# Optimization experiments

Hardware: AMD Instinct MI355X
Metric: run time of the kernel (lower is better)

The kernel has to match this reference:

```python
import jax, jax.numpy as jnp
from jax import lax
import numpy as np

B, L, V, E, D, T = 512, 200, 50000, 256, 256, 6
H = D // 2          # per-direction LSTM hidden
SLOPE = 0.01        # LeakyReLU negative slope
START, STOP = 4, 5  # tag_map['START'], tag_map['STOP']


def setup_inputs():
    key = jax.random.key(0)
    ks = jax.random.split(key, 18)
    w = lambda k, shape, scale=0.05: jax.random.normal(k, shape, jnp.float32) * scale
    trans = jax.random.normal(ks[17], (T, T), jnp.float32)
    trans = trans.at[:, START].set(-1000.0)
    trans = trans.at[STOP, :].set(-1000.0)
    return {
        "sentences": jax.random.randint(ks[0], (B, L), 0, V),
        "real_length": jnp.full((B,), L, dtype=jnp.int32),
        "emb": jax.random.normal(ks[1], (V, E), jnp.float32),
        "Wih_f": w(ks[2], (4 * H, E)), "Whh_f": w(ks[3], (4 * H, H)),
        "bih_f": w(ks[4], (4 * H,)),   "bhh_f": w(ks[5], (4 * H,)),
        "Wih_b": w(ks[6], (4 * H, E)), "Whh_b": w(ks[7], (4 * H, H)),
        "bih_b": w(ks[8], (4 * H,)),   "bhh_b": w(ks[9], (4 * H,)),
        "W1": w(ks[10], (D, D)), "b1": w(ks[11], (D,)),
        "W2": w(ks[12], (D, D)), "b2": w(ks[13], (D,)),
        "Wt": w(ks[14], (T, D)), "bt": w(ks[15], (T,)),
        "transitions": trans,
    }


def _leaky(x):
    return jnp.where(x >= 0, x, SLOPE * x)


def _lstm_dir(x, Wih, Whh, bih, bhh):
    # x: [B, L, E] -> hidden states [B, L, H]; PyTorch gate order i,f,g,o
    Bn = x.shape[0]
    Hn = Whh.shape[1]
    xg = jnp.einsum('ble,ge->blg', x, Wih) + bih + bhh  # [B, L, 4H]
    def step(carry, xt):
        h, c = carry
        g = xt + h @ Whh.T
        i, f, gg, o = jnp.split(g, 4, axis=-1)
        c = jax.nn.sigmoid(f) * c + jax.nn.sigmoid(i) * jnp.tanh(gg)
        h = jax.nn.sigmoid(o) * jnp.tanh(c)
        return (h, c), h
    init = (jnp.zeros((Bn, Hn), x.dtype), jnp.zeros((Bn, Hn), x.dtype))
    _, hs = lax.scan(step, init, jnp.swapaxes(xg, 0, 1))  # [L, B, H]
    return jnp.swapaxes(hs, 0, 1)


def _emissions(sentences, emb, Wih_f, Whh_f, bih_f, bhh_f, Wih_b, Whh_b, bih_b, bhh_b,
               W1, b1, W2, b2, Wt, bt):
    x = emb[sentences]                                   # [B, L, E]
    hf = _lstm_dir(x, Wih_f, Whh_f, bih_f, bhh_f)
    hb = _lstm_dir(x[:, ::-1], Wih_b, Whh_b, bih_b, bhh_b)[:, ::-1]
    h = jnp.concatenate([hf, hb], axis=-1)               # [B, L, D]
    h = _leaky(h @ W1.T + b1)
    h = _leaky(h @ W2.T + b2)
    return _leaky(h @ Wt.T + bt)                         # [B, L, T]


def _viterbi(logits, transitions):
    # logits: [L, T]; trellis recursion then backtrace
    def step(prev, obs):
        v = prev[:, None] + transitions                  # [T, T]
        tr = obs + jnp.max(v, axis=0)
        return tr, jnp.argmax(v, axis=0)
    last, bps = lax.scan(step, logits[0], logits[1:])    # bps: [L-1, T]
    score = jnp.max(last)
    last_tag = jnp.argmax(last)
    def back(tag, bp):
        new = bp[tag]
        return new, new
    _, prevs = lax.scan(back, last_tag, bps[::-1])
    path = jnp.concatenate([prevs[::-1], last_tag[None]])  # [L]
    return score, path


def reference(sentences, real_length, emb, Wih_f, Whh_f, bih_f, bhh_f,
              Wih_b, Whh_b, bih_b, bhh_b, W1, b1, W2, b2, Wt, bt, transitions):
    # real_length is full (=L) for every sample, so pack/pad is the identity,
    # matching the original forward's lengths=[i.size(-1)] behavior.
    logits = _emissions(sentences, emb, Wih_f, Whh_f, bih_f, bhh_f,
                        Wih_b, Whh_b, bih_b, bhh_b, W1, b1, W2, b2, Wt, bt)
    scores, paths = jax.vmap(_viterbi, in_axes=(0, None))(logits, transitions)
    return scores, paths
```

## Files before the change

### kernel.cpp

```cpp
#include <hip/hip_runtime.h>
#include <cmath>

#define B_   512
#define L_   200
#define V_   50000
#define E_   256
#define H_   128
#define G4H_ 512
#define D_   256
#define T_   6

__device__ __forceinline__ float sigmoidf_(float x) { return 1.0f / (1.0f + __expf(-x)); }
__device__ __forceinline__ float leakyf_(float x)   { return x >= 0.0f ? x : 0.01f * x; }

template<int CTRL>
__device__ __forceinline__ float dpp_add_(float x) {
    const int m = __builtin_amdgcn_mov_dpp(__float_as_int(x), CTRL, 0xF, 0xF, true);
    return x + __int_as_float(m);
}

#define XBM 128
#define XBN 128
#define XBK 8
#define XSTR 132

__global__ __launch_bounds__(256) void gemm_xg_chunk(
    const int* __restrict__ sent, const float* __restrict__ emb,
    const float* __restrict__ Wf, const float* __restrict__ Wb,
    const float* __restrict__ bihf, const float* __restrict__ bhhf,
    const float* __restrict__ bihb, const float* __restrict__ bhhb,
    float* __restrict__ xgc, int c0, int tc)
{
    __shared__ float As[2][XBK][XSTR];
    __shared__ float Bs[2][XBK][XSTR];
    __shared__ int   tok[XBM];

    const int bm  = blockIdx.x;
    const int bn  = blockIdx.y;
    const int tid = threadIdx.x;
    const int half = B_ * tc;
    const int dir  = (bm * XBM) >= half;

    if (tid < XBM) {
        const int vm  = bm * XBM + tid;
        const int rem = vm - dir * half;
        const int b   = rem / tc;
        const int ti  = rem - b * tc;
        const int s   = c0 + ti;
        const int t   = dir ? (L_ - 1 - s) : s;
        tok[tid] = sent[b * L_ + t];
    }
    __syncthreads();

    const int tx = tid & 15;
    const int ty = tid >> 4;
    const int n0 = bn * XBN;

    const float* W   = dir ? Wb   : Wf;
    const float* bih = dir ? bihb : bihf;
    const float* bhh = dir ? bhhb : bhhf;

    const int am = tid >> 1;
    const int ak = (tid & 1) * 4;

    const float* arow = emb + (size_t)tok[am] * E_ + ak;
    const float* brow = W + (size_t)(n0 + am) * E_ + ak;

    float acc[8][8];
#pragma unroll
    for (int i = 0; i < 8; ++i)
#pragma unroll
        for (int j = 0; j < 8; ++j) acc[i][j] = 0.0f;

    {
        const float4 a = *(const float4*)(arow);
        const float4 b = *(const float4*)(brow);
        As[0][ak + 0][am] = a.x; As[0][ak + 1][am] = a.y;
        As[0][ak + 2][am] = a.z; As[0][ak + 3][am] = a.w;
        Bs[0][ak + 0][am] = b.x; Bs[0][ak + 1][am] = b.y;
        Bs[0][ak + 2][am] = b.z; Bs[0][ak + 3][am] = b.w;
    }
    __syncthreads();

    const int NIT = E_ / XBK;
    for (int it = 0; it < NIT; ++it) {
        const int cur = it & 1;
        const int kn  = (it + 1) * XBK;
        float4 na, nb;
        if (kn < E_) {
            na = *(const float4*)(arow + kn);
            nb = *(const float4*)(brow + kn);
        }
#pragma unroll
        for (int k = 0; k < XBK; ++k) {
            float a[8], bb[8];
            *(float4*)a        = *(const float4*)&As[cur][k][ty * 4];
            *(float4*)(a + 4)  = *(const float4*)&As[cur][k][64 + ty * 4];
            *(float4*)(bb)     = *(const float4*)&Bs[cur][k][tx * 4];
            *(float4*)(bb + 4) = *(const float4*)&Bs[cur][k][64 + tx * 4];
#pragma unroll
            for (int i = 0; i < 8; ++i)
#pragma unroll
                for (int j = 0; j < 8; ++j) acc[i][j] += a[i] * bb[j];
        }
        if (kn < E_) {
            const int nxt = cur ^ 1;
            As[nxt][ak + 0][am] = na.x; As[nxt][ak + 1][am] = na.y;
            As[nxt][ak + 2][am] = na.z; As[nxt][ak + 3][am] = na.w;
            Bs[nxt][ak + 0][am] = nb.x; Bs[nxt][ak + 1][am] = nb.y;
            Bs[nxt][ak + 2][am] = nb.z; Bs[nxt][ak + 3][am] = nb.w;
        }
        __syncthreads();
    }

    const int nb0i = n0 + tx * 4;
    const int nb1i = n0 + 64 + tx * 4;
    float bias[8];
#pragma unroll
    for (int j = 0; j < 4; ++j) {
        bias[j]     = bih[nb0i + j] + bhh[nb0i + j];
        bias[4 + j] = bih[nb1i + j] + bhh[nb1i + j];
    }
#pragma unroll
    for (int i = 0; i < 8; ++i) {
        const int row = bm * XBM + ((i < 4) ? (ty * 4 + i) : (64 + ty * 4 + i - 4));
        float* dst = xgc + (size_t)row * G4H_;
        float4 v0, v1;
        v0.x = acc[i][0] + bias[0]; v0.y = acc[i][1] + bias[1];
        v0.z = acc[i][2] + bias[2]; v0.w = acc[i][3] + bias[3];
        v1.x = acc[i][4] + bias[4]; v1.y = acc[i][5] + bias[5];
        v1.z = acc[i][6] + bias[6]; v1.w = acc[i][7] + bias[7];
        *(float4*)(dst + nb0i) = v0;
        *(float4*)(dst + nb1i) = v1;
    }
}

__global__ __launch_bounds__(512, 2) void lstm_scan_chunk(
    const float* __restrict__ xgc,
    const float* __restrict__ Whh_f, const float* __restrict__ Whh_b,
    float* __restrict__ state, float* __restrict__ hcat, int c0, int tc)
{
    const int wg  = blockIdx.x;
    const int dir = wg >> 7;
    const int b0  = (wg & 127) * 4;
    const int tid = threadIdx.x;

    const int q  = tid & 3;
    const int g2 = tid >> 2;

    const float* Whh = dir ? Whh_b : Whh_f;

    float w[4][32];
#pragma unroll
    for (int p = 0; p < 4; ++p) {
        const float* wr = Whh + (size_t)(g2 + 128 * p) * H_ + q * 32;
#pragma unroll
        for (int kk = 0; kk < 32; kk += 4) {
            const float4 v = *(const float4*)(wr + kk);
            w[p][kk] = v.x; w[p][kk + 1] = v.y; w[p][kk + 2] = v.z; w[p][kk + 3] = v.w;
        }
    }

    __shared__ float hbuf[2][4 * 132];

    float c, hval;
    if (c0 == 0) {
        hval = 0.0f;
        c    = 0.0f;
    } else {
        hval = state[((size_t)(dir * B_ + b0 + q) * 2 + 0) * H_ + g2];
        c    = state[((size_t)(dir * B_ + b0 + q) * 2 + 1) * H_ + g2];
    }
    hbuf[0][(g2 >> 5) * 132 + (g2 & 31) * 4 + q] = hval;

    const int t0    = dir ? (L_ - 1 - c0) : c0;
    const int hstep = dir ? -D_ : D_;

    const float* xq = xgc + ((size_t)(dir * B_ + b0 + q) * tc) * G4H_ + g2;
    float* hp = hcat + ((size_t)(b0 + q) * L_ + t0) * D_ + dir * H_ + g2;

    __syncthreads();

    for (int t = 0; t < tc; ++t) {
        const int par = t & 1;
        const float* hq = &hbuf[par][q * 132];

        float xg[4];
#pragma unroll
        for (int p = 0; p < 4; ++p) xg[p] = xq[128 * p];
        xq += G4H_;

        float acc[4][4];
#pragma unroll
        for (int p = 0; p < 4; ++p)
#pragma unroll
            for (int s = 0; s < 4; ++s) acc[p][s] = 0.0f;

#pragma unroll
        for (int kk = 0; kk < 32; ++kk) {
            const float4 hv = *(const float4*)(hq + kk * 4);
#pragma unroll
            for (int p = 0; p < 4; ++p) {
                acc[p][0] += w[p][kk] * hv.x;
                acc[p][1] += w[p][kk] * hv.y;
                acc[p][2] += w[p][kk] * hv.z;
                acc[p][3] += w[p][kk] * hv.w;
            }
        }

#pragma unroll
        for (int p = 0; p < 4; ++p)
#pragma unroll
            for (int s = 0; s < 4; ++s) {
                float v = acc[p][s];
                v = dpp_add_<0xB1>(v);
                v = dpp_add_<0x4E>(v);
                acc[p][s] = v;
            }

        float gi = acc[0][0], gf = acc[1][0], gg = acc[2][0], go = acc[3][0];
        if (q == 1) { gi = acc[0][1]; gf = acc[1][1]; gg = acc[2][1]; go = acc[3][1]; }
        if (q == 2) { gi = acc[0][2]; gf = acc[1][2]; gg = acc[2][2]; go = acc[3][2]; }
        if (q == 3) { gi = acc[0][3]; gf = acc[1][3]; gg = acc[2][3]; go = acc[3][3]; }
        gi += xg[0]; gf += xg[1]; gg += xg[2]; go += xg[3];

        c    = sigmoidf_(gf) * c + sigmoidf_(gi) * tanhf(gg);
        hval = sigmoidf_(go) * tanhf(c);

        hbuf[par ^ 1][(g2 >> 5) * 132 + (g2 & 31) * 4 + q] = hval;
        hp[0] = hval;
        hp += hstep;
        __syncthreads();
    }

    state[((size_t)(dir * B_ + b0 + q) * 2 + 0) * H_ + g2] = hval;
    state[((size_t)(dir * B_ + b0 + q) * 2 + 1) * H_ + g2] = c;
}

#define BM 64
#define BN 128
#define BK 16
#define ASTR 68
#define BSTR 132
#define S1T 68

__global__ __launch_bounds__(256) void fused_mlp(
    const float* __restrict__ hcat,
    const float* __restrict__ W1, const float* __restrict__ b1,
    const float* __restrict__ W2, const float* __restrict__ b2,
    const float* __restrict__ Wt, const float* __restrict__ bt,
    float* __restrict__ logits)
{
    __shared__ float As[BK][ASTR];
    __shared__ float Bs[BK][BSTR];
    __shared__ float h1T[BN][S1T];
    __shared__ float Wt_s[T_][D_ + 2];
    __shared__ float b1_s[D_], b2_s[D_], bt_s[T_];

    const int tid  = threadIdx.x;
    const int row0 = blockIdx.x * BM;

    for (int i = tid; i < T_ * D_; i += 256) Wt_s[i >> 8][i & 255] = Wt[i];
    b1_s[tid] = b1[tid];
    b2_s[tid] = b2[tid];
    if (tid < T_) bt_s[tid] = bt[tid];

    const int tx = tid & 15;
    const int ty = tid >> 4;
    const int lrow = tid >> 2;
    const int lk   = (tid & 3) * 4;

    const float* arow = hcat + (size_t)(row0 + lrow) * D_ + lk;

    float acc2[2][4][8];
#pragma unroll
    for (int q = 0; q < 2; ++q)
#pragma unroll
        for (int i = 0; i < 4; ++i)
#pragma unroll
            for (int j = 0; j < 8; ++j) acc2[q][i][j] = 0.0f;

    for (int n0t = 0; n0t < 2; ++n0t) {
        const int n0 = n0t * BN;

        float acc1[4][8];
#pragma unroll
        for (int i = 0; i < 4; ++i)
#pragma unroll
            for (int j = 0; j < 8; ++j) acc1[i][j] = 0.0f;

        for (int k0 = 0; k0 < D_; k0 += BK) {
            {
                const float4 v = *(const float4*)(arow + k0);
                As[lk + 0][lrow] = v.x; As[lk + 1][lrow] = v.y;
                As[lk + 2][lrow] = v.z; As[lk + 3][lrow] = v.w;
            }
#pragma unroll
            for (int p = 0; p < 2; ++p) {
                const int n = p * 64 + lrow;
                const float4 v = *(const float4*)(W1 + (size_t)(n0 + n) * D_ + k0 + lk);
                Bs[lk + 0][n] = v.x; Bs[lk + 1][n] = v.y;
                Bs[lk + 2][n] = v.z; Bs[lk + 3][n] = v.w;
            }
            __syncthreads();
#pragma unroll
            for (int k = 0; k < BK; ++k) {
                float a[4], bb[8];
                *(float4*)a        = *(const float4*)&As[k][ty * 4];
                *(float4*)(bb)     = *(const float4*)&Bs[k][tx * 4];
                *(float4*)(bb + 4) = *(const float4*)&Bs[k][64 + tx * 4];
#pragma unroll
                for (int i = 0; i < 4; ++i)
#pragma unroll
                    for (int j = 0; j < 8; ++j) acc1[i][j] += a[i] * bb[j];
            }
            __syncthreads();
        }

#pragma unroll
        for (int j = 0; j < 8; ++j) {
            const int nl = (j < 4) ? (tx * 4 + j) : (64 + tx * 4 + j - 4);
            const float bv = b1_s[n0 + nl];
            float4 v;
            v.x = leakyf_(acc1[0][j] + bv);
            v.y = leakyf_(acc1[1][j] + bv);
            v.z = leakyf_(acc1[2][j] + bv);
            v.w = leakyf_(acc1[3][j] + bv);
            *(float4*)&h1T[nl][ty * 4] = v;
        }
        __syncthreads();

#pragma unroll
        for (int n2t = 0; n2t < 2; ++n2t) {
            for (int kc = 0; kc < BN; kc += BK) {
#pragma unroll
                for (int p = 0; p < 2; ++p) {
                    const int n = p * 64 + lrow;
                    const float4 v = *(const float4*)(W2 + (size_t)(n2t * BN + n) * D_ + n0 + kc + lk);
                    Bs[lk + 0][n] = v.x; Bs[lk + 1][n] = v.y;
                    Bs[lk + 2][n] = v.z; Bs[lk + 3][n] = v.w;
                }
                __syncthreads();
#pragma unroll
                for (int k = 0; k < BK; ++k) {
                    float a[4], bb[8];
                    *(float4*)a        = *(const float4*)&h1T[kc + k][ty * 4];
                    *(float4*)(bb)     = *(const float4*)&Bs[k][tx * 4];
                    *(float4*)(bb + 4) = *(const float4*)&Bs[k][64 + tx * 4];
#pragma unroll
                    for (int i = 0; i < 4; ++i)
#pragma unroll
                        for (int j = 0; j < 8; ++j) acc2[n2t][i][j] += a[i] * bb[j];
                }
                __syncthreads();
            }
        }
    }

    float part[4][T_];
#pragma unroll
    for (int i = 0; i < 4; ++i)
#pragma unroll
        for (int jt = 0; jt < T_; ++jt) part[i][jt] = 0.0f;

#pragma unroll
    for (int q = 0; q < 2; ++q)
#pragma unroll
        for (int j = 0; j < 8; ++j) {
            const int n = q * BN + ((j < 4) ? (tx * 4 + j) : (64 + tx * 4 + j - 4));
            const float bv = b2_s[n];
            float h2v[4];
#pragma unroll
            for (int i = 0; i < 4; ++i) h2v[i] = leakyf_(acc2[q][i][j] + bv);
#pragma unroll
            for (int jt = 0; jt < T_; ++jt) {
                const float wv = Wt_s[jt][n];
#pragma unroll
                for (int i = 0; i < 4; ++i) part[i][jt] += h2v[i] * wv;
            }
        }

#pragma unroll
    for (int m = 1; m <= 8; m <<= 1)
#pragma unroll
        for (int i = 0; i < 4; ++i)
#pragma unroll
            for (int jt = 0; jt < T_; ++jt)
                part[i][jt] += __shfl_xor(part[i][jt], m, 16);

    if (tx == 0) {
#pragma unroll
        for (int i = 0; i < 4; ++i) {
            const int m = row0 + ty * 4 + i;
#pragma unroll
            for (int jt = 0; jt < T_; ++jt)
                logits[(size_t)m * T_ + jt] = leakyf_(part[i][jt] + bt_s[jt]);
        }
    }
}

__global__ __launch_bounds__(64) void viterbi_kernel(
    const float* __restrict__ logits, const float* __restrict__ trans,
    float* __restrict__ out)
{
    const int b = blockIdx.x;
    const int lane = threadIdx.x;

    __shared__ unsigned char bp[L_][8];
    __shared__ int path_s[L_];

    float tr[T_];
    if (lane < T_) {
#pragma unroll
        for (int i = 0; i < T_; ++i) tr[i] = trans[i * T_ + lane];
    }
    const float* lg = logits + (size_t)b * L_ * T_;
    float prev = (lane < T_) ? lg[lane] : -1e30f;

    for (int t = 1; t < L_; ++t) {
        float m = -1e30f; int arg = 0;
#pragma unroll
        for (int i = 0; i < T_; ++i) {
            const float v = __shfl(prev, i, 64) + tr[i];
            if (v > m) { m = v; arg = i; }
        }
        const float obs = (lane < T_) ? lg[t * T_ + lane] : 0.0f;
        prev = obs + m;
        if (lane < T_) bp[t][lane] = (unsigned char)arg;
    }
    __syncthreads();

    float best = __shfl(prev, 0, 64); int tag = 0;
#pragma unroll
    for (int jj = 1; jj < T_; ++jj) {
        const float v = __shfl(prev, jj, 64);
        if (v > best) { best = v; tag = jj; }
    }
    if (lane == 0) {
        out[b] = best;
        path_s[L_ - 1] = tag;
        for (int t = L_ - 1; t >= 1; --t) {
            tag = bp[t][tag];
            path_s[t - 1] = tag;
        }
    }
    __syncthreads();
    for (int i = lane; i < L_; i += 64)
        out[B_ + (size_t)b * L_ + i] = (float)path_s[i];
}

extern "C" void kernel_launch(void* const* d_in, const int* in_sizes, int n_in,
                              void* d_out, int out_size, void* d_ws, size_t ws_size,
                              hipStream_t stream)
{
    (void)in_sizes; (void)n_in; (void)out_size;

    const int*   sent  = (const int*)  d_in[0];
    const float* emb   = (const float*)d_in[2];
    const float* Wih_f = (const float*)d_in[3];
    const float* Whh_f = (const float*)d_in[4];
    const float* bih_f = (const float*)d_in[5];
    const float* bhh_f = (const float*)d_in[6];
    const float* Wih_b = (const float*)d_in[7];
    const float* Whh_b = (const float*)d_in[8];
    const float* bih_b = (const float*)d_in[9];
    const float* bhh_b = (const float*)d_in[10];
    const float* W1    = (const float*)d_in[11];
    const float* b1    = (const float*)d_in[12];
    const float* W2    = (const float*)d_in[13];
    const float* b2    = (const float*)d_in[14];
    const float* Wt    = (const float*)d_in[15];
    const float* bt    = (const float*)d_in[16];
    const float* trans = (const float*)d_in[17];

    float* ws = (float*)d_ws;
    const size_t HCAT_E = (size_t)B_ * L_ * D_;
    const size_t LG_E   = (size_t)B_ * L_ * T_;
    const size_t ST_E   = (size_t)2 * B_ * 2 * H_;
    float* hcat   = ws;
    float* logits = ws + HCAT_E;
    float* state  = logits + LG_E;
    float* xgc    = state + ST_E;

    const size_t base  = HCAT_E + LG_E + ST_E;
    const size_t per_t = (size_t)2 * B_ * G4H_;
    const size_t ws_f  = ws_size / sizeof(float);
    long long avail = (long long)ws_f - (long long)base;
    int Tc = (avail > 0) ? (int)(avail / (long long)per_t) : 0;
    if (Tc < 1)  Tc = 1;
    if (Tc > L_) Tc = L_;

    float* out = (float*)d_out;

    for (int c0 = 0; c0 < L_; c0 += Tc) {
        const int tc = (L_ - c0 < Tc) ? (L_ - c0) : Tc;
        gemm_xg_chunk<<<dim3(8 * tc, 4), 256, 0, stream>>>(
            sent, emb, Wih_f, Wih_b, bih_f, bhh_f, bih_b, bhh_b, xgc, c0, tc);
        lstm_scan_chunk<<<256, 512, 0, stream>>>(
            xgc, Whh_f, Whh_b, state, hcat, c0, tc);
    }
    fused_mlp<<<(B_ * L_) / BM, 256, 0, stream>>>(
        hcat, W1, b1, W2, b2, Wt, bt, logits);
    viterbi_kernel<<<B_, 64, 0, stream>>>(logits, trans, out);
}
```

Baseline: 1.816 ms.

## Split fused MLP into register-tiled GEMM plus fused second-layer/tag-projection kernel

Replaces the single fused MLP kernel with two kernels when there is enough workspace. The first is a 128x128 double-buffered, 8x8 register-tiled GEMM computing the first layer with bias and LeakyReLU into a scratch buffer that reuses the xg chunk area. The second runs the second layer GEMM and folds in the 6-way tag projection, using shuffle reductions. This trades an extra full-size intermediate write and read for larger, more efficient GEMM tiles. The old fused path is kept as a fallback.

```diff
diff --git a/kernel.cpp b/kernel.cpp
--- a/kernel.cpp
+++ b/kernel.cpp
@@ -235,6 +235,214 @@
 
     state[((size_t)(dir * B_ + b0 + q) * 2 + 0) * H_ + g2] = hval;
     state[((size_t)(dir * B_ + b0 + q) * 2 + 1) * H_ + g2] = c;
+}
+
+__global__ __launch_bounds__(256) void mlp1_gemm(
+    const float* __restrict__ hcat,
+    const float* __restrict__ W1, const float* __restrict__ b1,
+    float* __restrict__ h1)
+{
+    __shared__ float As[2][XBK][XSTR];
+    __shared__ float Bs[2][XBK][XSTR];
+
+    const int bm  = blockIdx.x;
+    const int bn  = blockIdx.y;
+    const int tid = threadIdx.x;
+    const int tx = tid & 15;
+    const int ty = tid >> 4;
+    const int n0 = bn * XBN;
+
+    const int am = tid >> 1;
+    const int ak = (tid & 1) * 4;
+
+    const float* arow = hcat + (size_t)(bm * XBM + am) * D_ + ak;
+    const float* brow = W1 + (size_t)(n0 + am) * D_ + ak;
+
+    float acc[8][8];
+#pragma unroll
+    for (int i = 0; i < 8; ++i)
+#pragma unroll
+        for (int j = 0; j < 8; ++j) acc[i][j] = 0.0f;
+
+    {
+        const float4 a = *(const float4*)(arow);
+        const float4 b = *(const float4*)(brow);
+        As[0][ak + 0][am] = a.x; As[0][ak + 1][am] = a.y;
+        As[0][ak + 2][am] = a.z; As[0][ak + 3][am] = a.w;
+        Bs[0][ak + 0][am] = b.x; Bs[0][ak + 1][am] = b.y;
+        Bs[0][ak + 2][am] = b.z; Bs[0][ak + 3][am] = b.w;
+    }
+    __syncthreads();
+
+    const int NIT = D_ / XBK;
+    for (int it = 0; it < NIT; ++it) {
+        const int cur = it & 1;
+        const int kn  = (it + 1) * XBK;
+        float4 na, nb;
+        if (kn < D_) {
+            na = *(const float4*)(arow + kn);
+            nb = *(const float4*)(brow + kn);
+        }
+#pragma unroll
+        for (int k = 0; k < XBK; ++k) {
+            float a[8], bb[8];
+            *(float4*)a        = *(const float4*)&As[cur][k][ty * 4];
+            *(float4*)(a + 4)  = *(const float4*)&As[cur][k][64 + ty * 4];
+            *(float4*)(bb)     = *(const float4*)&Bs[cur][k][tx * 4];
+            *(float4*)(bb + 4) = *(const float4*)&Bs[cur][k][64 + tx * 4];
+#pragma unroll
+            for (int i = 0; i < 8; ++i)
+#pragma unroll
+                for (int j = 0; j < 8; ++j) acc[i][j] += a[i] * bb[j];
+        }
+        if (kn < D_) {
+            const int nxt = cur ^ 1;
+            As[nxt][ak + 0][am] = na.x; As[nxt][ak + 1][am] = na.y;
+            As[nxt][ak + 2][am] = na.z; As[nxt][ak + 3][am] = na.w;
+            Bs[nxt][ak + 0][am] = nb.x; Bs[nxt][ak + 1][am] = nb.y;
+            Bs[nxt][ak + 2][am] = nb.z; Bs[nxt][ak + 3][am] = nb.w;
+        }
+        __syncthreads();
+    }
+
+    const int nb0i = n0 + tx * 4;
+    const int nb1i = n0 + 64 + tx * 4;
+    float bias[8];
+#pragma unroll
+    for (int j = 0; j < 4; ++j) {
+        bias[j]     = b1[nb0i + j];
+        bias[4 + j] = b1[nb1i + j];
+    }
+#pragma unroll
+    for (int i = 0; i < 8; ++i) {
+        const int row = bm * XBM + ((i < 4) ? (ty * 4 + i) : (64 + ty * 4 + i - 4));
+        float* dst = h1 + (size_t)row * D_;
+        float4 v0, v1;
+        v0.x = leakyf_(acc[i][0] + bias[0]); v0.y = leakyf_(acc[i][1] + bias[1]);
+        v0.z = leakyf_(acc[i][2] + bias[2]); v0.w = leakyf_(acc[i][3] + bias[3]);
+        v1.x = leakyf_(acc[i][4] + bias[4]); v1.y = leakyf_(acc[i][5] + bias[5]);
+        v1.z = leakyf_(acc[i][6] + bias[6]); v1.w = leakyf_(acc[i][7] + bias[7]);
+        *(float4*)(dst + nb0i) = v0;
+        *(float4*)(dst + nb1i) = v1;
+    }
+}
+
+__global__ __launch_bounds__(256) void mlp2tag(
+    const float* __restrict__ h1,
+    const float* __restrict__ W2, const float* __restrict__ b2,
+    const float* __restrict__ Wt, const float* __restrict__ bt,
+    float* __restrict__ logits)
+{
+    __shared__ float As[2][XBK][XSTR];
+    __shared__ float Bs[2][XBK][XSTR];
+    __shared__ float Wt_s[T_][D_ + 2];
+    __shared__ float b2_s[D_];
+    __shared__ float bt_s[T_];
+
+    const int bm  = blockIdx.x;
+    const int tid = threadIdx.x;
+    const int tx = tid & 15;
+    const int ty = tid >> 4;
+
+    for (int i = tid; i < T_ * D_; i += 256) Wt_s[i >> 8][i & 255] = Wt[i];
+    b2_s[tid] = b2[tid];
+    if (tid < T_) bt_s[tid] = bt[tid];
+
+    const int am = tid >> 1;
+    const int ak = (tid & 1) * 4;
+
+    const float* arow = h1 + (size_t)(bm * XBM + am) * D_ + ak;
+
+    float part[8][T_];
+#pragma unroll
+    for (int i = 0; i < 8; ++i)
+#pragma unroll
+        for (int jt = 0; jt < T_; ++jt) part[i][jt] = 0.0f;
+
+    for (int n0t = 0; n0t < 2; ++n0t) {
+        const int n0 = n0t * XBN;
+        const float* brow = W2 + (size_t)(n0 + am) * D_ + ak;
+
+        float acc[8][8];
+#pragma unroll
+        for (int i = 0; i < 8; ++i)
+#pragma unroll
+            for (int j = 0; j < 8; ++j) acc[i][j] = 0.0f;
+
+        {
+            const float4 a = *(const float4*)(arow);
+            const float4 b = *(const float4*)(brow);
+            As[0][ak + 0][am] = a.x; As[0][ak + 1][am] = a.y;
+            As[0][ak + 2][am] = a.z; As[0][ak + 3][am] = a.w;
+            Bs[0][ak + 0][am] = b.x; Bs[0][ak + 1][am] = b.y;
+            Bs[0][ak + 2][am] = b.z; Bs[0][ak + 3][am] = b.w;
+        }
+        __syncthreads();
+
+        const int NIT = D_ / XBK;
+        for (int it = 0; it < NIT; ++it) {
+            const int cur = it & 1;
+            const int kn  = (it + 1) * XBK;
+            float4 na, nb;
+            if (kn < D_) {
+                na = *(const float4*)(arow + kn);
+                nb = *(const float4*)(brow + kn);
+            }
+#pragma unroll
+            for (int k = 0; k < XBK; ++k) {
+                float a[8], bb[8];
+                *(float4*)a        = *(const float4*)&As[cur][k][ty * 4];
+                *(float4*)(a + 4)  = *(const float4*)&As[cur][k][64 + ty * 4];
+                *(float4*)(bb)     = *(const float4*)&Bs[cur][k][tx * 4];
+                *(float4*)(bb + 4) = *(const float4*)&Bs[cur][k][64 + tx * 4];
+#pragma unroll
+                for (int i = 0; i < 8; ++i)
+#pragma unroll
+                    for (int j = 0; j < 8; ++j) acc[i][j] += a[i] * bb[j];
+            }
+            if (kn < D_) {
+                const int nxt = cur ^ 1;
+                As[nxt][ak + 0][am] = na.x; As[nxt][ak + 1][am] = na.y;
+                As[nxt][ak + 2][am] = na.z; As[nxt][ak + 3][am] = na.w;
+                Bs[nxt][ak + 0][am] = nb.x; Bs[nxt][ak + 1][am] = nb.y;
+                Bs[nxt][ak + 2][am] = nb.z; Bs[nxt][ak + 3][am] = nb.w;
+            }
+            __syncthreads();
+        }
+
+#pragma unroll
+        for (int j = 0; j < 8; ++j) {
+            const int col = n0 + ((j < 4) ? (tx * 4 + j) : (64 + tx * 4 + j - 4));
+            const float bv = b2_s[col];
+            float h2v[8];
+#pragma unroll
+            for (int i = 0; i < 8; ++i) h2v[i] = leakyf_(acc[i][j] + bv);
+#pragma unroll
+            for (int jt = 0; jt < T_; ++jt) {
+                const float wv = Wt_s[jt][col];
+#pragma unroll
+                for (int i = 0; i < 8; ++i) part[i][jt] += h2v[i] * wv;
+            }
+        }
+    }
+
+#pragma unroll
+    for (int m = 1; m <= 8; m <<= 1)
+#pragma unroll
+        for (int i = 0; i < 8; ++i)
+#pragma unroll
+            for (int jt = 0; jt < T_; ++jt)
+                part[i][jt] += __shfl_xor(part[i][jt], m, 16);
+
+    if (tx == 0) {
+#pragma unroll
+        for (int i = 0; i < 8; ++i) {
+            const int row = bm * XBM + ((i < 4) ? (ty * 4 + i) : (64 + ty * 4 + i - 4));
+#pragma unroll
+            for (int jt = 0; jt < T_; ++jt)
+                logits[(size_t)row * T_ + jt] = leakyf_(part[i][jt] + bt_s[jt]);
+        }
+    }
 }
 
 #define BM 64
@@ -477,6 +685,7 @@
     const size_t HCAT_E = (size_t)B_ * L_ * D_;
     const size_t LG_E   = (size_t)B_ * L_ * T_;
     const size_t ST_E   = (size_t)2 * B_ * 2 * H_;
+    const size_t H1_E   = HCAT_E;
     float* hcat   = ws;
     float* logits = ws + HCAT_E;
     float* state  = logits + LG_E;
@@ -499,7 +708,14 @@
         lstm_scan_chunk<<<256, 512, 0, stream>>>(
             xgc, Whh_f, Whh_b, state, hcat, c0, tc);
     }
-    fused_mlp<<<(B_ * L_) / BM, 256, 0, stream>>>(
-        hcat, W1, b1, W2, b2, Wt, bt, logits);
+
+    if (avail >= (long long)H1_E) {
+        float* h1 = xgc;
+        mlp1_gemm<<<dim3((B_ * L_) / XBM, 2), 256, 0, stream>>>(hcat, W1, b1, h1);
+        mlp2tag<<<(B_ * L_) / XBM, 256, 0, stream>>>(h1, W2, b2, Wt, bt, logits);
+    } else {
+        fused_mlp<<<(B_ * L_) / BM, 256, 0, stream>>>(
+            hcat, W1, b1, W2, b2, Wt, bt, logits);
+    }
     viterbi_kernel<<<B_, 64, 0, stream>>>(logits, trans, out);
 }
```

After: 1.822 ms. No clear change (+0.3%).

## Split LSTM recurrent dot products across eight lanes using 1024-thread blocks

Applied to the files above, without the earlier changes.

The recurrent scan kernel now splits each gate's 128-element hidden dot product across 8 lanes of 16 elements instead of 4 lanes of 32. Block size doubles to 1024 threads, and an extra DPP half-row mirror step completes the cross-lane reduction. Because the scan is a serial, latency-bound recurrence, halving per-thread FMA work per timestep should shorten each step's critical path. In exchange, the extra reduction step adds cost, half the lanes sit idle during the gate nonlinearities and stores, and the weight register footprint is reshaped.

```diff
diff --git a/kernel.cpp b/kernel.cpp
--- a/kernel.cpp
+++ b/kernel.cpp
@@ -135,7 +135,7 @@
     }
 }
 
-__global__ __launch_bounds__(512, 2) void lstm_scan_chunk(
+__global__ __launch_bounds__(1024) void lstm_scan_chunk(
     const float* __restrict__ xgc,
     const float* __restrict__ Whh_f, const float* __restrict__ Whh_b,
     float* __restrict__ state, float* __restrict__ hcat, int c0, int tc)
@@ -145,49 +145,50 @@
     const int b0  = (wg & 127) * 4;
     const int tid = threadIdx.x;
 
-    const int q  = tid & 3;
-    const int g2 = tid >> 2;
+    const int e   = tid & 7;
+    const int g2  = tid >> 3;
+    const int sx  = e & 3;
 
     const float* Whh = dir ? Whh_b : Whh_f;
 
-    float w[4][32];
+    float w[4][16];
 #pragma unroll
     for (int p = 0; p < 4; ++p) {
-        const float* wr = Whh + (size_t)(g2 + 128 * p) * H_ + q * 32;
-#pragma unroll
-        for (int kk = 0; kk < 32; kk += 4) {
+        const float* wr = Whh + (size_t)(g2 + 128 * p) * H_ + e * 16;
+#pragma unroll
+        for (int kk = 0; kk < 16; kk += 4) {
             const float4 v = *(const float4*)(wr + kk);
             w[p][kk] = v.x; w[p][kk + 1] = v.y; w[p][kk + 2] = v.z; w[p][kk + 3] = v.w;
         }
     }
 
-    __shared__ float hbuf[2][4 * 132];
-
-    float c, hval;
-    if (c0 == 0) {
-        hval = 0.0f;
-        c    = 0.0f;
-    } else {
-        hval = state[((size_t)(dir * B_ + b0 + q) * 2 + 0) * H_ + g2];
-        c    = state[((size_t)(dir * B_ + b0 + q) * 2 + 1) * H_ + g2];
-    }
-    hbuf[0][(g2 >> 5) * 132 + (g2 & 31) * 4 + q] = hval;
+    __shared__ float hbuf[2][8 * 68];
+
+    float c = 0.0f, hval = 0.0f;
+    if (e < 4) {
+        if (c0 != 0) {
+            hval = state[((size_t)(dir * B_ + b0 + e) * 2 + 0) * H_ + g2];
+            c    = state[((size_t)(dir * B_ + b0 + e) * 2 + 1) * H_ + g2];
+        }
+        hbuf[0][(g2 >> 4) * 68 + (g2 & 15) * 4 + e] = hval;
+    }
 
     const int t0    = dir ? (L_ - 1 - c0) : c0;
     const int hstep = dir ? -D_ : D_;
 
-    const float* xq = xgc + ((size_t)(dir * B_ + b0 + q) * tc) * G4H_ + g2;
-    float* hp = hcat + ((size_t)(b0 + q) * L_ + t0) * D_ + dir * H_ + g2;
+    const float* xq = xgc + ((size_t)(dir * B_ + b0 + sx) * tc) * G4H_ + g2;
+    float* hp = hcat + ((size_t)(b0 + sx) * L_ + t0) * D_ + dir * H_ + g2;
 
     __syncthreads();
 
     for (int t = 0; t < tc; ++t) {
         const int par = t & 1;
-        const float* hq = &hbuf[par][q * 132];
-
-        float xg[4];
-#pragma unroll
-        for (int p = 0; p < 4; ++p) xg[p] = xq[128 * p];
+        const float* hq = &hbuf[par][e * 68];
+
+        float xg0 = 0.f, xg1 = 0.f, xg2v = 0.f, xg3 = 0.f;
+        if (e < 4) {
+            xg0 = xq[0]; xg1 = xq[128]; xg2v = xq[256]; xg3 = xq[384];
+        }
         xq += G4H_;
 
         float acc[4][4];
@@ -197,7 +198,7 @@
             for (int s = 0; s < 4; ++s) acc[p][s] = 0.0f;
 
 #pragma unroll
-        for (int kk = 0; kk < 32; ++kk) {
+        for (int kk = 0; kk < 16; ++kk) {
             const float4 hv = *(const float4*)(hq + kk * 4);
 #pragma unroll
             for (int p = 0; p < 4; ++p) {
@@ -215,26 +216,31 @@
                 float v = acc[p][s];
                 v = dpp_add_<0xB1>(v);
                 v = dpp_add_<0x4E>(v);
+                v = dpp_add_<0x141>(v);
                 acc[p][s] = v;
             }
 
-        float gi = acc[0][0], gf = acc[1][0], gg = acc[2][0], go = acc[3][0];
-        if (q == 1) { gi = acc[0][1]; gf = acc[1][1]; gg = acc[2][1]; go = acc[3][1]; }
-        if (q == 2) { gi = acc[0][2]; gf = acc[1][2]; gg = acc[2][2]; go = acc[3][2]; }
-        if (q == 3) { gi = acc[0][3]; gf = acc[1][3]; gg = acc[2][3]; go = acc[3][3]; }
-        gi += xg[0]; gf += xg[1]; gg += xg[2]; go += xg[3];
-
-        c    = sigmoidf_(gf) * c + sigmoidf_(gi) * tanhf(gg);
-        hval = sigmoidf_(go) * tanhf(c);
-
-        hbuf[par ^ 1][(g2 >> 5) * 132 + (g2 & 31) * 4 + q] = hval;
-        hp[0] = hval;
+        if (e < 4) {
+            float gi = acc[0][0], gf = acc[1][0], gg = acc[2][0], go = acc[3][0];
+            if (e == 1) { gi = acc[0][1]; gf = acc[1][1]; gg = acc[2][1]; go = acc[3][1]; }
+            if (e == 2) { gi = acc[0][2]; gf = acc[1][2]; gg = acc[2][2]; go = acc[3][2]; }
+            if (e == 3) { gi = acc[0][3]; gf = acc[1][3]; gg = acc[2][3]; go = acc[3][3]; }
+            gi += xg0; gf += xg1; gg += xg2v; go += xg3;
+
+            c    = sigmoidf_(gf) * c + sigmoidf_(gi) * tanhf(gg);
+            hval = sigmoidf_(go) * tanhf(c);
+
+            hbuf[par ^ 1][(g2 >> 4) * 68 + (g2 & 15) * 4 + e] = hval;
+            hp[0] = hval;
+        }
         hp += hstep;
         __syncthreads();
     }
 
-    state[((size_t)(dir * B_ + b0 + q) * 2 + 0) * H_ + g2] = hval;
-    state[((size_t)(dir * B_ + b0 + q) * 2 + 1) * H_ + g2] = c;
+    if (e < 4) {
+        state[((size_t)(dir * B_ + b0 + e) * 2 + 0) * H_ + g2] = hval;
+        state[((size_t)(dir * B_ + b0 + e) * 2 + 1) * H_ + g2] = c;
+    }
 }
 
 #define BM 64
@@ -496,7 +502,7 @@
         const int tc = (L_ - c0 < Tc) ? (L_ - c0) : Tc;
         gemm_xg_chunk<<<dim3(8 * tc, 4), 256, 0, stream>>>(
             sent, emb, Wih_f, Wih_b, bih_f, bhh_f, bih_b, bhh_b, xgc, c0, tc);
-        lstm_scan_chunk<<<256, 512, 0, stream>>>(
+        lstm_scan_chunk<<<256, 1024, 0, stream>>>(
             xgc, Whh_f, Whh_b, state, hcat, c0, tc);
     }
     fused_mlp<<<(B_ * L_) / BM, 256, 0, stream>>>(
```

Result: slower. 2.041 ms (+12.4%).
